# Kernel tuning notes

Measured on AMD Instinct MI355X. Metric: run time of the kernel, lower is better.

The kernel has to match this reference:

```python
import jax, jax.numpy as jnp
import numpy as np

B, T = 512, 16385  # batch, num_samples; fitted window M = T - 1


def setup_inputs() -> dict:
    key = jax.random.key(0)
    k1, _ = jax.random.split(key)
    # positive samples so ny + cumsum(x) stays > 0 (needed for u**r and log u)
    x = jax.random.uniform(k1, (B, 1, T), dtype=jnp.float32)
    params = jnp.array([0.5, 1.0], dtype=jnp.float32)  # [r, ny]
    return {"x": x, "params": params}


def _cusum(x, h):
    # trapezoidal cumulative integral: y[0]=0, y[t]=y[t-1]+0.5*h*(x[t-1]+x[t])
    inc = 0.5 * h * (x[..., :-1] + x[..., 1:])
    zero = jnp.zeros(x.shape[:-1] + (1,), x.dtype)
    return jnp.concatenate([zero, jnp.cumsum(inc, axis=-1)], axis=-1)


def reference(x, params):
    r, ny = params[0], params[1]
    y = _cusum(x, 1.0)              # (B, 1, T)
    u = ny + y[:, 0, 1:]            # (B, M) ; M = T-1
    phi = jnp.stack([u, u ** r], axis=1)   # (B, 2, M) basis
    phip = jnp.linalg.pinv(phi)            # (B, M, 2)
    xd = x[:, :, 1:]                        # (B, 1, M)
    coeffs = xd @ phip                      # (B, 1, 2)
    x_hat = coeffs @ phi                    # (B, 1, M)
    res = xd - x_hat                        # (B, 1, M)
    r2 = jnp.sum(res ** 2, axis=-1)         # (B, 1)
    return coeffs, x_hat, res, r2
```

## Files before the change

### kernel.cpp

```cpp
#include <hip/hip_runtime.h>
#include <hip/hip_bf16.h>

#define TPB 256
#define VPT 8
#define TILE (TPB * VPT)
#define NDAT 16384
#define NTILES (NDAT / TILE)
#define TLEN 16385

__global__ __launch_bounds__(TPB) void vpl_kernel(
    const float* __restrict__ x, const float* __restrict__ params,
    float* __restrict__ out, int B) {
  const int b = blockIdx.x;
  const int tid = threadIdx.x;
  const int lane = tid & 63;
  const int wid = tid >> 6;

  const float r = params[0];
  const float ny = params[1];
  const bool rhalf = (r == 0.5f);

  const float* __restrict__ xr = x + (size_t)b * TLEN;

  float* out_coeffs = out;
  float* out_xhat = out + (size_t)2 * B + (size_t)b * NDAT;
  float* out_res = out + (size_t)2 * B + (size_t)B * NDAT + (size_t)b * NDAT;
  float* out_r2 = out + (size_t)2 * B + (size_t)2 * B * NDAT;

  __shared__ float wt[4];
  __shared__ double sred[4][5];
  __shared__ float cbc[2];

  double carry = 0.0;
  double s_u = 0.0, s_u2 = 0.0, s_u15 = 0.0, s_xu = 0.0, s_xv = 0.0;

  for (int k = 0; k < NTILES; ++k) {
    const int base = k * TILE + tid * VPT;
    float xs[VPT + 1];
#pragma unroll
    for (int j = 0; j <= VPT; ++j) xs[j] = xr[base + j];

    float run[VPT];
    float acc = 0.f;
#pragma unroll
    for (int j = 0; j < VPT; ++j) {
      acc += 0.5f * (xs[j] + xs[j + 1]);
      run[j] = acc;
    }
    const float total = acc;

    float t = total;
#pragma unroll
    for (int d = 1; d < 64; d <<= 1) {
      float o = __shfl_up(t, d, 64);
      if (lane >= d) t += o;
    }
    if (lane == 63) wt[wid] = t;
    __syncthreads();

    float woff = 0.f, ttot = 0.f;
#pragma unroll
    for (int w = 0; w < 4; ++w) {
      float v = wt[w];
      ttot += v;
      if (w < wid) woff += v;
    }
    const float pre = woff + (t - total);
    const double ubase = carry + (double)ny;

    float uu[VPT];
#pragma unroll
    for (int j = 0; j < VPT; ++j) {
      const double ud = ubase + (double)(pre + run[j]);
      uu[j] = (float)ud;
      const double v = rhalf ? sqrt(ud) : pow(ud, (double)r);
      const double xd = (double)xs[j + 1];
      s_u += ud;
      s_u2 += ud * ud;
      s_u15 += ud * v;
      s_xu += xd * ud;
      s_xv += xd * v;
    }
    *reinterpret_cast<float4*>(out_res + base) =
        make_float4(uu[0], uu[1], uu[2], uu[3]);
    *reinterpret_cast<float4*>(out_res + base + 4) =
        make_float4(uu[4], uu[5], uu[6], uu[7]);

    carry += (double)ttot;
    __syncthreads();
  }

  {
    double vals[5] = {s_u, s_u2, s_u15, s_xu, s_xv};
#pragma unroll
    for (int i = 0; i < 5; ++i) {
      double v = vals[i];
#pragma unroll
      for (int d = 32; d >= 1; d >>= 1) v += __shfl_down(v, d, 64);
      vals[i] = v;
    }
    if (lane == 0) {
#pragma unroll
      for (int i = 0; i < 5; ++i) sred[wid][i] = vals[i];
    }
  }
  __syncthreads();

  if (tid == 0) {
    double g[5];
#pragma unroll
    for (int i = 0; i < 5; ++i)
      g[i] = sred[0][i] + sred[1][i] + sred[2][i] + sred[3][i];
    const double g11 = g[0];
    const double g00 = g[1];
    const double g01 = g[2];
    const double b0 = g[3];
    const double b1 = g[4];

    const double tr = g00 + g11;
    const double det = g00 * g11 - g01 * g01;
    const double disc = sqrt(fmax(tr * tr - 4.0 * det, 0.0));
    const double l1 = 0.5 * (tr + disc);
    const double l2 = (l1 > 0.0) ? fmax(det / l1, 0.0) : 0.0;
    const double s1 = sqrt(fmax(l1, 0.0));
    const double s2 = sqrt(l2);
    const double rcond = 0.01953125;

    double c0, c1;
    if (s2 > rcond * s1) {
      c0 = (g11 * b0 - g01 * b1) / det;
      c1 = (g00 * b1 - g01 * b0) / det;
    } else if (s1 > 0.0) {
      double w0 = l1 - g11, w1 = g01;
      double nrm = sqrt(w0 * w0 + w1 * w1);
      double e0, e1;
      if (nrm > 0.0) {
        e0 = w0 / nrm;
        e1 = w1 / nrm;
      } else {
        e0 = 1.0;
        e1 = 0.0;
      }
      const double gam = (b0 * e0 + b1 * e1) / l1;
      c0 = gam * e0;
      c1 = gam * e1;
    } else {
      c0 = 0.0;
      c1 = 0.0;
    }
    out_coeffs[2 * b] = (float)c0;
    out_coeffs[2 * b + 1] = (float)c1;
    cbc[0] = (float)c0;
    cbc[1] = (float)c1;
  }
  __syncthreads();
  const float c0 = cbc[0];
  const float c1 = cbc[1];

  double r2 = 0.0;
  for (int k = 0; k < NTILES; ++k) {
    const int base = k * TILE + tid * VPT;
    const float4 u0 = *reinterpret_cast<const float4*>(out_res + base);
    const float4 u1v = *reinterpret_cast<const float4*>(out_res + base + 4);
    float uu[VPT] = {u0.x, u0.y, u0.z, u0.w, u1v.x, u1v.y, u1v.z, u1v.w};
    float xd[VPT];
#pragma unroll
    for (int j = 0; j < VPT; ++j) xd[j] = xr[base + 1 + j];

    float xh[VPT], rs[VPT];
#pragma unroll
    for (int j = 0; j < VPT; ++j) {
      const float vh = rhalf ? sqrtf(uu[j]) : powf(uu[j], r);
      xh[j] = c0 * uu[j] + c1 * vh;
      rs[j] = xd[j] - xh[j];
      r2 += (double)rs[j] * (double)rs[j];
    }
    *reinterpret_cast<float4*>(out_xhat + base) =
        make_float4(xh[0], xh[1], xh[2], xh[3]);
    *reinterpret_cast<float4*>(out_xhat + base + 4) =
        make_float4(xh[4], xh[5], xh[6], xh[7]);
    *reinterpret_cast<float4*>(out_res + base) =
        make_float4(rs[0], rs[1], rs[2], rs[3]);
    *reinterpret_cast<float4*>(out_res + base + 4) =
        make_float4(rs[4], rs[5], rs[6], rs[7]);
  }

#pragma unroll
  for (int d = 32; d >= 1; d >>= 1) r2 += __shfl_down(r2, d, 64);
  if (lane == 0) sred[wid][0] = r2;
  __syncthreads();
  if (tid == 0)
    out_r2[b] = (float)(sred[0][0] + sred[1][0] + sred[2][0] + sred[3][0]);
}

extern "C" void kernel_launch(void* const* d_in, const int* in_sizes, int n_in,
                              void* d_out, int out_size, void* d_ws,
                              size_t ws_size, hipStream_t stream) {
  const float* x = (const float*)d_in[0];
  const float* params = (const float*)d_in[1];
  float* out = (float*)d_out;
  const int B = in_sizes[0] / TLEN;
  vpl_kernel<<<dim3(B), dim3(TPB), 0, stream>>>(x, params, out, B);
}
```

Baseline: 113.1 us.

## Recompute cumulative sum in second pass instead of staging u through global memory

Drops the write of u into the residual buffer during the first pass and the read-back in the second. The second pass instead rereads x and recomputes the local trapezoid prefix using per-tile double offsets kept in registers. It also raises the block size from 256 to 1024 threads, giving two tiles per row with fully unrolled loops and one fewer barrier. The cost is extra recompute, higher register pressure, and only one 1024-thread block per row, which may limit occupancy.

After: 110.2 us. 1.03x faster.

```diff
diff --git a/kernel.cpp b/kernel.cpp
--- a/kernel.cpp
+++ b/kernel.cpp
@@ -1,12 +1,13 @@
 #include <hip/hip_runtime.h>
 #include <hip/hip_bf16.h>
 
-#define TPB 256
+#define TPB 1024
 #define VPT 8
 #define TILE (TPB * VPT)
 #define NDAT 16384
 #define NTILES (NDAT / TILE)
 #define TLEN 16385
+#define NWAVES (TPB / 64)
 
 __global__ __launch_bounds__(TPB) void vpl_kernel(
     const float* __restrict__ x, const float* __restrict__ params,
@@ -27,13 +28,15 @@
   float* out_res = out + (size_t)2 * B + (size_t)B * NDAT + (size_t)b * NDAT;
   float* out_r2 = out + (size_t)2 * B + (size_t)2 * B * NDAT;
 
-  __shared__ float wt[4];
-  __shared__ double sred[4][5];
+  __shared__ float wt[NWAVES];
+  __shared__ double sred[NWAVES][5];
   __shared__ float cbc[2];
 
   double carry = 0.0;
+  double off[NTILES];
   double s_u = 0.0, s_u2 = 0.0, s_u15 = 0.0, s_xu = 0.0, s_xv = 0.0;
 
+#pragma unroll
   for (int k = 0; k < NTILES; ++k) {
     const int base = k * TILE + tid * VPT;
     float xs[VPT + 1];
@@ -60,19 +63,17 @@
 
     float woff = 0.f, ttot = 0.f;
 #pragma unroll
-    for (int w = 0; w < 4; ++w) {
+    for (int w = 0; w < NWAVES; ++w) {
       float v = wt[w];
       ttot += v;
       if (w < wid) woff += v;
     }
     const float pre = woff + (t - total);
-    const double ubase = carry + (double)ny;
-
-    float uu[VPT];
+    off[k] = carry + (double)ny + (double)pre;
+
 #pragma unroll
     for (int j = 0; j < VPT; ++j) {
-      const double ud = ubase + (double)(pre + run[j]);
-      uu[j] = (float)ud;
+      const double ud = off[k] + (double)run[j];
       const double v = rhalf ? sqrt(ud) : pow(ud, (double)r);
       const double xd = (double)xs[j + 1];
       s_u += ud;
@@ -81,13 +82,8 @@
       s_xu += xd * ud;
       s_xv += xd * v;
     }
-    *reinterpret_cast<float4*>(out_res + base) =
-        make_float4(uu[0], uu[1], uu[2], uu[3]);
-    *reinterpret_cast<float4*>(out_res + base + 4) =
-        make_float4(uu[4], uu[5], uu[6], uu[7]);
-
     carry += (double)ttot;
-    __syncthreads();
+    if (k + 1 < NTILES) __syncthreads();
   }
 
   {
@@ -109,8 +105,12 @@
   if (tid == 0) {
     double g[5];
 #pragma unroll
-    for (int i = 0; i < 5; ++i)
-      g[i] = sred[0][i] + sred[1][i] + sred[2][i] + sred[3][i];
+    for (int i = 0; i < 5; ++i) {
+      double s = 0.0;
+#pragma unroll
+      for (int w = 0; w < NWAVES; ++w) s += sred[w][i];
+      g[i] = s;
+    }
     const double g11 = g[0];
     const double g00 = g[1];
     const double g01 = g[2];
@@ -158,21 +158,22 @@
   const float c1 = cbc[1];
 
   double r2 = 0.0;
+#pragma unroll
   for (int k = 0; k < NTILES; ++k) {
     const int base = k * TILE + tid * VPT;
-    const float4 u0 = *reinterpret_cast<const float4*>(out_res + base);
-    const float4 u1v = *reinterpret_cast<const float4*>(out_res + base + 4);
-    float uu[VPT] = {u0.x, u0.y, u0.z, u0.w, u1v.x, u1v.y, u1v.z, u1v.w};
-    float xd[VPT];
-#pragma unroll
-    for (int j = 0; j < VPT; ++j) xd[j] = xr[base + 1 + j];
-
+    float xs[VPT + 1];
+#pragma unroll
+    for (int j = 0; j <= VPT; ++j) xs[j] = xr[base + j];
+
+    float acc = 0.f;
     float xh[VPT], rs[VPT];
 #pragma unroll
     for (int j = 0; j < VPT; ++j) {
-      const float vh = rhalf ? sqrtf(uu[j]) : powf(uu[j], r);
-      xh[j] = c0 * uu[j] + c1 * vh;
-      rs[j] = xd[j] - xh[j];
+      acc += 0.5f * (xs[j] + xs[j + 1]);
+      const float uu = (float)(off[k] + (double)acc);
+      const float vh = rhalf ? sqrtf(uu) : powf(uu, r);
+      xh[j] = c0 * uu + c1 * vh;
+      rs[j] = xs[j + 1] - xh[j];
       r2 += (double)rs[j] * (double)rs[j];
     }
     *reinterpret_cast<float4*>(out_xhat + base) =
@@ -189,8 +190,12 @@
   for (int d = 32; d >= 1; d >>= 1) r2 += __shfl_down(r2, d, 64);
   if (lane == 0) sred[wid][0] = r2;
   __syncthreads();
-  if (tid == 0)
-    out_r2[b] = (float)(sred[0][0] + sred[1][0] + sred[2][0] + sred[3][0]);
+  if (tid == 0) {
+    double s = 0.0;
+#pragma unroll
+    for (int w = 0; w < NWAVES; ++w) s += sred[w][0];
+    out_r2[b] = (float)s;
+  }
 }
 
 extern "C" void kernel_launch(void* const* d_in, const int* in_sizes, int n_in,
```
